# Optimization experiments

Hardware: AMD Instinct MI355X
Metric: run time of the kernel (lower is better)

The kernel has to match this reference:

```python
import jax, jax.numpy as jnp
import numpy as np

TEMP_LEN = 16
TARGET_LEN = 22
DIM = 768
HEADS = 12
B = 16
NT = TEMP_LEN * TEMP_LEN          # 256 template tokens
NG = TARGET_LEN * TARGET_LEN      # 484 target tokens
N = NT + NG                       # 740
POS_HID = 512


def _gaussian_heatmap(center, size, sig=1.0):
    x_axis = np.linspace(0, size[0] - 1, size[0]) - center[0]
    y_axis = np.linspace(0, size[1] - 1, size[1]) - center[1]
    xx, yy = np.meshgrid(x_axis, y_axis)
    return np.exp(-0.5 * (xx ** 2 + yy ** 2) / sig ** 2)


def _bias_index(L):
    # faithful to getBiasIndex (w_len == h_len here)
    coords = np.stack(np.meshgrid(np.arange(L), np.arange(L), indexing='ij'))  # [2,L,L]
    flat = coords.reshape(2, -1)                                               # [2,L*L]
    rel = (flat[:, :, None] - flat[:, None, :]).transpose(1, 2, 0).astype(np.int64)
    rel[:, :, 0] += L - 1
    rel[:, :, 1] += L - 1
    rel[:, :, 0] *= 2 * L - 1
    return rel.sum(-1)  # [L*L, L*L]


def setup_inputs() -> dict:
    key = jax.random.key(0)
    ks = jax.random.split(key, 12)
    f32 = jnp.float32
    x = jax.random.normal(ks[0], (B, N, DIM), dtype=f32)
    temp_q = jax.random.normal(ks[1], (B, NT, DIM), dtype=f32)
    target_q = jax.random.normal(ks[2], (B, NG, DIM), dtype=f32)
    # linear weights stored [in, out] (transposed torch layout)
    w = lambda k, i, o: jax.random.normal(k, (i, o), dtype=f32) * 0.02
    q_w = w(ks[3], DIM, DIM)
    k_w = w(ks[4], DIM, DIM)
    v_w = w(ks[5], DIM, DIM)
    proj_w = w(ks[6], DIM, DIM)
    proj_b = jnp.zeros((DIM,), dtype=f32)
    rpb_table = jax.random.normal(ks[7], ((2 * TARGET_LEN - 1) ** 2, HEADS), dtype=f32) * 0.0002
    rpb_table_temp = jax.random.normal(ks[8], ((2 * TEMP_LEN - 1) ** 2, HEADS), dtype=f32) * 0.0002
    pos_w1 = w(ks[9], 2, POS_HID)
    pos_b1 = jnp.zeros((POS_HID,), dtype=f32)
    pos_w2 = w(ks[10], POS_HID, HEADS)
    pos_b2 = jnp.zeros((HEADS,), dtype=f32)
    # deterministic cross-bias coordinate table (non-learned buffer)
    temp_tab = _gaussian_heatmap((TEMP_LEN // 2, TEMP_LEN // 2), (TEMP_LEN, TEMP_LEN)).astype(np.float32).flatten() \
        + np.linspace(-0.2, 0.2, NT, dtype=np.float32)
    targ_tab = _gaussian_heatmap((TARGET_LEN // 2, TARGET_LEN // 2), (TARGET_LEN, TARGET_LEN)).astype(np.float32).flatten() \
        + np.linspace(-0.2, 0.2, NG, dtype=np.float32)
    # torch.meshgrid default indexing='ij': [2, NT, NG] -> permute(1,2,0) -> [NT,NG,2]
    temp_target = np.stack(np.meshgrid(temp_tab, targ_tab, indexing='ij')).transpose(1, 2, 0)
    target_temp_tab = jnp.asarray(temp_target.transpose(1, 0, 2))  # [NG, NT, 2]
    temp_idx = jnp.asarray(_bias_index(TEMP_LEN))       # [NT, NT] int64
    target_idx = jnp.asarray(_bias_index(TARGET_LEN))   # [NG, NG] int64
    return {
        'x': x, 'temp_q': temp_q, 'target_q': target_q,
        'q_w': q_w, 'k_w': k_w, 'v_w': v_w, 'proj_w': proj_w, 'proj_b': proj_b,
        'rpb_table': rpb_table, 'rpb_table_temp': rpb_table_temp,
        'pos_w1': pos_w1, 'pos_b1': pos_b1, 'pos_w2': pos_w2, 'pos_b2': pos_b2,
        'target_temp_tab': target_temp_tab,
        'temp_idx': temp_idx, 'target_idx': target_idx,
    }


def reference(x, temp_q, target_q, q_w, k_w, v_w, proj_w, proj_b,
              rpb_table, rpb_table_temp, pos_w1, pos_b1, pos_w2, pos_b2,
              target_temp_tab, temp_idx, target_idx):
    Bsz, Ntok, C = x.shape
    H = HEADS
    hd = C // H
    scale = hd ** -0.5

    q_in = jnp.concatenate([temp_q, target_q], axis=1)                 # [B,N,C]
    q = (q_in @ q_w).reshape(Bsz, Ntok, H, hd).transpose(0, 2, 1, 3)   # [B,H,N,hd]
    k = (x @ k_w).reshape(Bsz, Ntok, H, hd).transpose(0, 2, 1, 3)
    v = (x @ v_w).reshape(Bsz, Ntok, H, hd).transpose(0, 2, 1, 3)

    # gathered relative position biases -> [H, Ni, Ni]
    temp_rpb = rpb_table_temp[temp_idx.reshape(-1)].reshape(NT, NT, H).transpose(2, 0, 1)
    targ_rpb = rpb_table[target_idx.reshape(-1)].reshape(NG, NG, H).transpose(2, 0, 1)
    # MLP cross bias: [NG, NT, 2] -> [NG, NT, H] -> [H, NG, NT]
    hid = jax.nn.relu(target_temp_tab @ pos_w1 + pos_b1)
    target_temp_bias = (hid @ pos_w2 + pos_b2).transpose(2, 0, 1)      # [H,NG,NT]
    temp_target_bias = target_temp_bias.transpose(0, 2, 1)             # [H,NT,NG]
    top = jnp.concatenate([temp_rpb, temp_target_bias], axis=2)        # [H,NT,N]
    bot = jnp.concatenate([target_temp_bias, targ_rpb], axis=2)        # [H,NG,N]
    bias = jnp.concatenate([top, bot], axis=1)[None]                   # [1,H,N,N]

    attn = jnp.einsum('bhnd,bhmd->bhnm', q, k) * scale + bias
    attn = jax.nn.softmax(attn, axis=-1)
    out = jnp.einsum('bhnm,bhmd->bhnd', attn, v).transpose(0, 2, 1, 3).reshape(Bsz, Ntok, C)
    return out @ proj_w + proj_b
```

## Files before the change

kernel.cpp:

```cpp
#include <hip/hip_runtime.h>


typedef unsigned short u16;
typedef short bf16x8 __attribute__((ext_vector_type(8)));
typedef float f32x4 __attribute__((ext_vector_type(4)));

#define BSZ   16
#define NTOK  740
#define NTMP  256
#define NTGT  484
#define DIMC  768
#define NHEAD 12
#define HDIM  64
#define MROWS (BSZ*NTOK)
#define SMAX  16.0f
#define VSTR  66

__device__ __forceinline__ float bf2f(u16 u) {
    return __uint_as_float(((unsigned int)u) << 16);
}
__device__ __forceinline__ float bflo(unsigned int u) {
    return __uint_as_float(u << 16);
}
__device__ __forceinline__ float bfhi(unsigned int u) {
    return __uint_as_float(u & 0xffff0000u);
}
__device__ __forceinline__ u16 f2bf(float f) {
    unsigned int u = __float_as_uint(f);
    u += 0x7fffu + ((u >> 16) & 1u);
    return (u16)(u >> 16);
}

__device__ __forceinline__ void gl_lds16(const u16* g, u16* l) {
    __builtin_amdgcn_global_load_lds(
        (const __attribute__((address_space(1))) unsigned int*)(unsigned long long)g,
        (__attribute__((address_space(3))) unsigned int*)(unsigned int)(unsigned long long)l,
        16, 0, 0);
}

__device__ __forceinline__ size_t b2off(int h, int i, int j) {
    return ((size_t)(h * NTOK + i)) * 768 + ((j >> 6) << 6) + ((j & 15) << 2) + ((j >> 4) & 3);
}

__global__ __launch_bounds__(256) void convert_qx(
    const float* __restrict__ x, const float* __restrict__ tq,
    const float* __restrict__ gq, u16* __restrict__ XB, u16* __restrict__ QB)
{
    int c = blockIdx.x * 256 + threadIdx.x;
    if (c >= MROWS * DIMC / 8) return;
    {
        const float* s = x + (size_t)c * 8;
        float4 p0 = *(const float4*)s, p1 = *(const float4*)(s + 4);
        u16 e[8] = {f2bf(p0.x), f2bf(p0.y), f2bf(p0.z), f2bf(p0.w),
                    f2bf(p1.x), f2bf(p1.y), f2bf(p1.z), f2bf(p1.w)};
        *(uint4*)(XB + (size_t)c * 8) = *(uint4*)e;
    }
    {
        int row = c / 96, cc = (c - row * 96) * 8;
        int b = row / NTOK, n = row - b * NTOK;
        const float* s = (n < NTMP)
                       ? tq + ((size_t)(b * NTMP + n)) * DIMC + cc
                       : gq + ((size_t)(b * NTGT + (n - NTMP))) * DIMC + cc;
        float4 p0 = *(const float4*)s, p1 = *(const float4*)(s + 4);
        u16 e[8] = {f2bf(p0.x), f2bf(p0.y), f2bf(p0.z), f2bf(p0.w),
                    f2bf(p1.x), f2bf(p1.y), f2bf(p1.z), f2bf(p1.w)};
        *(uint4*)(QB + (size_t)row * DIMC + cc) = *(uint4*)e;
    }
}

__global__ __launch_bounds__(256) void transpose_w(
    const float* __restrict__ w0, const float* __restrict__ w1,
    const float* __restrict__ w2, const float* __restrict__ w3,
    u16* __restrict__ Wt)
{
    __shared__ float T[64][65];
    const float* src = (blockIdx.z == 0) ? w0 : (blockIdx.z == 1) ? w1
                     : (blockIdx.z == 2) ? w2 : w3;
    const float scale = (blockIdx.z == 0) ? 0.125f : 1.0f;
    u16* dst = Wt + (size_t)blockIdx.z * DIMC * DIMC;
    int out0 = blockIdx.x * 64, in0 = blockIdx.y * 64;
    int tid = threadIdx.x;
    #pragma unroll
    for (int l = 0; l < 4; l++) {
        int u = tid + (l << 8);
        int r = u >> 4, c4 = (u & 15) << 2;
        float4 p = *(const float4*)(src + (size_t)(in0 + r) * DIMC + out0 + c4);
        T[r][c4] = p.x; T[r][c4 + 1] = p.y; T[r][c4 + 2] = p.z; T[r][c4 + 3] = p.w;
    }
    __syncthreads();
    #pragma unroll
    for (int l = 0; l < 2; l++) {
        int u = tid + (l << 8);
        int r = u >> 3, c8 = (u & 7) << 3;
        u16 e[8];
        #pragma unroll
        for (int i = 0; i < 8; i++) e[i] = f2bf(T[c8 + i][r] * scale);
        *(uint4*)(dst + (size_t)(out0 + r) * DIMC + in0 + c8) = *(uint4*)e;
    }
}

__global__ __launch_bounds__(256) void bias_diag(
    const float* __restrict__ rpb, const float* __restrict__ rpbt,
    const int* __restrict__ tidx, const int* __restrict__ gidx,
    u16* __restrict__ bias)
{
    int j = blockIdx.x * 256 + threadIdx.x;
    int i = blockIdx.y;
    if (j >= 768) return;
    u16 vals[NHEAD];
    if (j >= NTOK) {
        u16 neg = f2bf(-1e30f);
        #pragma unroll
        for (int h = 0; h < NHEAD; h++) vals[h] = neg;
    } else if (i < NTMP && j < NTMP) {
        int idx = tidx[i * NTMP + j];
        #pragma unroll
        for (int h = 0; h < NHEAD; h++) vals[h] = f2bf(rpbt[idx * NHEAD + h]);
    } else if (i >= NTMP && j >= NTMP) {
        int idx = gidx[(i - NTMP) * NTGT + (j - NTMP)];
        #pragma unroll
        for (int h = 0; h < NHEAD; h++) vals[h] = f2bf(rpb[idx * NHEAD + h]);
    } else {
        return;
    }
    #pragma unroll
    for (int h = 0; h < NHEAD; h++) bias[b2off(h, i, j)] = vals[h];
}

__global__ __launch_bounds__(256) void bias_cross(
    const float* __restrict__ w1, const float* __restrict__ b1,
    const float* __restrict__ w2, const float* __restrict__ b2,
    const float* __restrict__ tab, u16* __restrict__ bias)
{
    int g = blockIdx.x, t = threadIdx.x;
    float a  = tab[(g * NTMP + t) * 2 + 0];
    float bb = tab[(g * NTMP + t) * 2 + 1];
    float acc[NHEAD];
    #pragma unroll
    for (int h = 0; h < NHEAD; h++) acc[h] = b2[h];
    for (int k = 0; k < 512; k++) {
        float hid = fmaxf(a * w1[k] + bb * w1[512 + k] + b1[k], 0.0f);
        #pragma unroll
        for (int h = 0; h < NHEAD; h++) acc[h] += hid * w2[k * NHEAD + h];
    }
    #pragma unroll
    for (int h = 0; h < NHEAD; h++) {
        u16 v = f2bf(acc[h]);
        bias[b2off(h, t, NTMP + g)] = v;
        bias[b2off(h, NTMP + g, t)] = v;
    }
}

template<int MODE>
__global__ __launch_bounds__(256) void gemm_bf16(
    const u16* __restrict__ A, const u16* __restrict__ Wt,
    const float* __restrict__ pb, u16* __restrict__ C0,
    u16* __restrict__ C1, float* __restrict__ Cf)
{
    __shared__ __align__(16) u16 As[8192];
    __shared__ __align__(16) u16 Bs[8192];
    const int tid = threadIdx.x;
    const int lane = tid & 63, w = tid >> 6;
    const int quad = lane >> 4, ln = lane & 15;
    const int m0 = blockIdx.y << 7, n0g = blockIdx.x << 7;
    const int wm = (w >> 1) << 6, wn = (w & 1) << 6;
    const u16* Wbase = Wt + (size_t)n0g * DIMC;

    f32x4 acc[4][4];
    #pragma unroll
    for (int i = 0; i < 4; i++)
        #pragma unroll
        for (int j = 0; j < 4; j++)
            acc[i][j] = (f32x4){0.f, 0.f, 0.f, 0.f};

    for (int k0 = 0; k0 < DIMC; k0 += 64) {
        __syncthreads();
        #pragma unroll
        for (int l = 0; l < 4; l++) {
            int f = tid + (l << 8);
            int c8 = f >> 7, r = f & 127;
            int grow = m0 + r; if (grow >= MROWS) grow = MROWS - 1;
            gl_lds16(A + (size_t)grow * DIMC + k0 + c8 * 8, As + f * 8);
            gl_lds16(Wbase + (size_t)r * DIMC + k0 + c8 * 8, Bs + f * 8);
        }
        __syncthreads();
        #pragma unroll
        for (int kp = 0; kp < 2; kp++) {
            bf16x8 af[4], bfr[4];
            #pragma unroll
            for (int mt = 0; mt < 4; mt++)
                af[mt] = *(const bf16x8*)&As[(((kp << 2) + quad) * 128 + wm + mt * 16 + ln) * 8];
            #pragma unroll
            for (int nt = 0; nt < 4; nt++)
                bfr[nt] = *(const bf16x8*)&Bs[(((kp << 2) + quad) * 128 + wn + nt * 16 + ln) * 8];
            #pragma unroll
            for (int mt = 0; mt < 4; mt++)
                #pragma unroll
                for (int nt = 0; nt < 4; nt++)
                    acc[mt][nt] = __builtin_amdgcn_mfma_f32_16x16x32_bf16(
                        af[mt], bfr[nt], acc[mt][nt], 0, 0, 0);
        }
    }

    u16* Cb = C0;
    int col0 = n0g;
    if (MODE == 1 && n0g >= DIMC) { Cb = C1; col0 = n0g - DIMC; }

    #pragma unroll
    for (int mt = 0; mt < 4; mt++) {
        #pragma unroll
        for (int reg = 0; reg < 4; reg++) {
            int grow = m0 + wm + mt * 16 + (quad << 2) + reg;
            if (grow >= MROWS) continue;
            #pragma unroll
            for (int nt = 0; nt < 4; nt++) {
                int gcol = col0 + wn + nt * 16 + ln;
                float v = acc[mt][nt][reg];
                if (MODE == 2) {
                    Cf[(size_t)grow * DIMC + gcol] = v + pb[gcol];
                } else {
                    Cb[(size_t)grow * DIMC + gcol] = f2bf(v);
                }
            }
        }
    }
}

__global__ __launch_bounds__(256) void attn_mfma(
    const u16* __restrict__ Qg, const u16* __restrict__ Kg,
    const u16* __restrict__ Vg, const u16* __restrict__ bias,
    u16* __restrict__ ctx)
{
    __shared__ __align__(16) u16 KsL[4096];
    __shared__ __align__(16) u16 VtL[64 * VSTR];
    __shared__ __align__(16) u16 Pw[8][16][72];

    const int tid = threadIdx.x;
    const int lane = tid & 63, w = tid >> 6;
    const int quad = lane >> 4, ln = lane & 15;
    const int b = blockIdx.z, h = blockIdx.y;
    const int q0 = blockIdx.x << 7;
    const int mbase = q0 + (w << 5);
    const u16* bp = bias + ((size_t)h * NTOK) * 768;

    bf16x8 aq[2][2];
    #pragma unroll
    for (int mi = 0; mi < 2; mi++) {
        int qrow = mbase + (mi << 4) + ln; if (qrow >= NTOK) qrow = NTOK - 1;
        #pragma unroll
        for (int kp = 0; kp < 2; kp++)
            aq[mi][kp] = *(const bf16x8*)(Qg + ((size_t)(b * NTOK + qrow)) * DIMC
                                          + h * HDIM + kp * 32 + (quad << 3));
    }
    int boff[2][4];
    #pragma unroll
    for (int mi = 0; mi < 2; mi++)
        #pragma unroll
        for (int reg = 0; reg < 4; reg++) {
            int rr = mbase + (mi << 4) + (quad << 2) + reg;
            if (rr >= NTOK) rr = NTOK - 1;
            boff[mi][reg] = rr * 768 + (ln << 2);
        }

    float rs[2][4] = {};
    f32x4 O[2][4];
    #pragma unroll
    for (int mi = 0; mi < 2; mi++)
        #pragma unroll
        for (int dt = 0; dt < 4; dt++) O[mi][dt] = (f32x4){0.f, 0.f, 0.f, 0.f};

    for (int j0 = 0; j0 < NTOK; j0 += 64) {
        __syncthreads();
        #pragma unroll
        for (int l = 0; l < 2; l++) {
            int f = tid + (l << 8);
            int chunk = f >> 6, jr = f & 63;
            int krow = j0 + jr; if (krow >= NTOK) krow = NTOK - 1;
            gl_lds16(Kg + ((size_t)(b * NTOK + krow)) * DIMC + h * HDIM + chunk * 8,
                     KsL + f * 8);
        }
        uint2 bvv[2][4];
        #pragma unroll
        for (int mi = 0; mi < 2; mi++)
            #pragma unroll
            for (int reg = 0; reg < 4; reg++)
                bvv[mi][reg] = *(const uint2*)(bp + boff[mi][reg] + j0);
        #pragma unroll
        for (int l = 0; l < 2; l++) {
            int u = tid + (l << 8);
            int jr = u >> 3, d0 = (u & 7) << 3;
            int vrow = j0 + jr; if (vrow >= NTOK) vrow = NTOK - 1;
            uint4 p = *(const uint4*)(Vg + ((size_t)(b * NTOK + vrow)) * DIMC + h * HDIM + d0);
            const u16* pe = (const u16*)&p;
            #pragma unroll
            for (int i = 0; i < 8; i++) VtL[(d0 + i) * VSTR + jr] = pe[i];
        }
        __syncthreads();

        bf16x8 bv[4][2];
        #pragma unroll
        for (int dt = 0; dt < 4; dt++)
            #pragma unroll
            for (int kp = 0; kp < 2; kp++) {
                const unsigned int* vp = (const unsigned int*)
                    &VtL[(dt * 16 + ln) * VSTR + kp * 32 + (quad << 3)];
                uint4 vv; vv.x = vp[0]; vv.y = vp[1]; vv.z = vp[2]; vv.w = vp[3];
                bv[dt][kp] = *(const bf16x8*)&vv;
            }

        #pragma unroll
        for (int mi = 0; mi < 2; mi++) {
            f32x4 s[4];
            #pragma unroll
            for (int nt = 0; nt < 4; nt++) {
                f32x4 c = (f32x4){0.f, 0.f, 0.f, 0.f};
                #pragma unroll
                for (int kp = 0; kp < 2; kp++) {
                    bf16x8 bk = *(const bf16x8*)
                        &KsL[(((kp << 2) + quad) * 64 + nt * 16 + ln) * 8];
                    c = __builtin_amdgcn_mfma_f32_16x16x32_bf16(aq[mi][kp], bk, c, 0, 0, 0);
                }
                s[nt] = c;
            }
            #pragma unroll
            for (int reg = 0; reg < 4; reg++) {
                uint2 bb = bvv[mi][reg];
                float p0 = __expf(s[0][reg] + bflo(bb.x) - SMAX);
                float p1 = __expf(s[1][reg] + bfhi(bb.x) - SMAX);
                float p2 = __expf(s[2][reg] + bflo(bb.y) - SMAX);
                float p3 = __expf(s[3][reg] + bfhi(bb.y) - SMAX);
                s[0][reg] = p0; s[1][reg] = p1; s[2][reg] = p2; s[3][reg] = p3;
                rs[mi][reg] += p0 + p1 + p2 + p3;
            }
            #pragma unroll
            for (int nt = 0; nt < 4; nt++)
                #pragma unroll
                for (int reg = 0; reg < 4; reg++)
                    Pw[(w << 1) + mi][(quad << 2) + reg][nt * 16 + ln] = f2bf(s[nt][reg]);
            bf16x8 ap[2];
            #pragma unroll
            for (int kp = 0; kp < 2; kp++)
                ap[kp] = *(const bf16x8*)&Pw[(w << 1) + mi][ln][kp * 32 + (quad << 3)];
            #pragma unroll
            for (int dt = 0; dt < 4; dt++)
                #pragma unroll
                for (int kp = 0; kp < 2; kp++)
                    O[mi][dt] = __builtin_amdgcn_mfma_f32_16x16x32_bf16(
                        ap[kp], bv[dt][kp], O[mi][dt], 0, 0, 0);
        }
    }

    #pragma unroll
    for (int mi = 0; mi < 2; mi++) {
        #pragma unroll
        for (int reg = 0; reg < 4; reg++) {
            float t = rs[mi][reg];
            #pragma unroll
            for (int mk = 8; mk >= 1; mk >>= 1) t += __shfl_xor(t, mk);
            float inv = 1.0f / t;
            int row = mbase + (mi << 4) + (quad << 2) + reg;
            if (row < NTOK) {
                #pragma unroll
                for (int dt = 0; dt < 4; dt++)
                    ctx[((size_t)(b * NTOK + row)) * DIMC + h * HDIM + dt * 16 + ln]
                        = f2bf(O[mi][dt][reg] * inv);
            }
        }
    }
}

extern "C" void kernel_launch(void* const* d_in, const int* in_sizes, int n_in,
                              void* d_out, int out_size, void* d_ws, size_t ws_size,
                              hipStream_t stream)
{
    const float* x        = (const float*)d_in[0];
    const float* temp_q   = (const float*)d_in[1];
    const float* target_q = (const float*)d_in[2];
    const float* q_w      = (const float*)d_in[3];
    const float* k_w      = (const float*)d_in[4];
    const float* v_w      = (const float*)d_in[5];
    const float* proj_w   = (const float*)d_in[6];
    const float* proj_b   = (const float*)d_in[7];
    const float* rpb      = (const float*)d_in[8];
    const float* rpbt     = (const float*)d_in[9];
    const float* pw1      = (const float*)d_in[10];
    const float* pb1      = (const float*)d_in[11];
    const float* pw2      = (const float*)d_in[12];
    const float* pb2      = (const float*)d_in[13];
    const float* tab      = (const float*)d_in[14];
    const int*   tidx     = (const int*)d_in[15];
    const int*   gidx     = (const int*)d_in[16];
    float* out = (float*)d_out;

    char* ws = (char*)d_ws;
    const size_t S = (size_t)MROWS * DIMC * sizeof(u16);
    const size_t SZB = (size_t)NHEAD * NTOK * 768 * sizeof(u16);
    u16* XB    = (u16*)(ws);
    u16* QB    = (u16*)(ws + S);
    u16* Q     = (u16*)(ws + 2 * S);
    u16* K     = (u16*)(ws + 3 * S);
    u16* V     = QB;
    u16* CTX   = XB;
    u16* BIAS2 = (u16*)(ws + 4 * S);
    u16* WT    = (u16*)(ws + 4 * S + SZB);

    convert_qx<<<dim3(4440), 256, 0, stream>>>(x, temp_q, target_q, XB, QB);
    transpose_w<<<dim3(12, 12, 4), 256, 0, stream>>>(q_w, k_w, v_w, proj_w, WT);
    bias_diag<<<dim3(3, 740), 256, 0, stream>>>(rpb, rpbt, tidx, gidx, BIAS2);
    bias_cross<<<dim3(484), 256, 0, stream>>>(pw1, pb1, pw2, pb2, tab, BIAS2);

    const u16* WTq = WT;
    const u16* WTkv = WT + (size_t)DIMC * DIMC;
    const u16* WTp = WT + 3 * (size_t)DIMC * DIMC;

    gemm_bf16<0><<<dim3(6, 93), 256, 0, stream>>>(QB, WTq, nullptr, Q, nullptr, nullptr);
    gemm_bf16<1><<<dim3(12, 93), 256, 0, stream>>>(XB, WTkv, nullptr, K, V, nullptr);
    attn_mfma<<<dim3(6, 12, 16), 256, 0, stream>>>(Q, K, V, BIAS2, CTX);
    gemm_bf16<2><<<dim3(6, 93), 256, 0, stream>>>(CTX, WTp, proj_b, nullptr, nullptr, out);
}
```

Measured before the change: 506.4 us.

## Fuse prep kernels, swizzle attention LDS layouts, and batch QK MFMAs

Merges the four preprocessing kernels (input conversion, weight transpose, diagonal bias, cross bias MLP) into one launch, with block ranges picking the job. In the attention kernel, the V-transpose and P staging buffers get XOR-swizzled layouts so reads can be single 16-byte vector loads without bank conflicts. QK^T is also computed for both row tiles together so each K fragment load feeds two MFMAs. The GEMM output-pointer selection moves before the main loop. The fused prep kernel may have uneven block workloads, and the swizzle math adds some index arithmetic.

```diff
diff --git a/kernel.cpp b/kernel.cpp
--- a/kernel.cpp
+++ b/kernel.cpp
@@ -14,7 +14,6 @@
 #define HDIM  64
 #define MROWS (BSZ*NTOK)
 #define SMAX  16.0f
-#define VSTR  66
 
 __device__ __forceinline__ float bf2f(u16 u) {
     return __uint_as_float(((unsigned int)u) << 16);
@@ -42,112 +41,113 @@
     return ((size_t)(h * NTOK + i)) * 768 + ((j >> 6) << 6) + ((j & 15) << 2) + ((j >> 4) & 3);
 }
 
-__global__ __launch_bounds__(256) void convert_qx(
+#define PREP_CONV 4440
+#define PREP_TRW  (PREP_CONV + 576)
+#define PREP_DIAG (PREP_TRW + 2220)
+#define PREP_ALL  (PREP_DIAG + 484)
+
+__global__ __launch_bounds__(256) void prep_kernel(
     const float* __restrict__ x, const float* __restrict__ tq,
-    const float* __restrict__ gq, u16* __restrict__ XB, u16* __restrict__ QB)
-{
-    int c = blockIdx.x * 256 + threadIdx.x;
-    if (c >= MROWS * DIMC / 8) return;
-    {
-        const float* s = x + (size_t)c * 8;
-        float4 p0 = *(const float4*)s, p1 = *(const float4*)(s + 4);
-        u16 e[8] = {f2bf(p0.x), f2bf(p0.y), f2bf(p0.z), f2bf(p0.w),
-                    f2bf(p1.x), f2bf(p1.y), f2bf(p1.z), f2bf(p1.w)};
-        *(uint4*)(XB + (size_t)c * 8) = *(uint4*)e;
-    }
-    {
-        int row = c / 96, cc = (c - row * 96) * 8;
-        int b = row / NTOK, n = row - b * NTOK;
-        const float* s = (n < NTMP)
-                       ? tq + ((size_t)(b * NTMP + n)) * DIMC + cc
-                       : gq + ((size_t)(b * NTGT + (n - NTMP))) * DIMC + cc;
-        float4 p0 = *(const float4*)s, p1 = *(const float4*)(s + 4);
-        u16 e[8] = {f2bf(p0.x), f2bf(p0.y), f2bf(p0.z), f2bf(p0.w),
-                    f2bf(p1.x), f2bf(p1.y), f2bf(p1.z), f2bf(p1.w)};
-        *(uint4*)(QB + (size_t)row * DIMC + cc) = *(uint4*)e;
-    }
-}
-
-__global__ __launch_bounds__(256) void transpose_w(
+    const float* __restrict__ gq, u16* __restrict__ XB, u16* __restrict__ QB,
     const float* __restrict__ w0, const float* __restrict__ w1,
     const float* __restrict__ w2, const float* __restrict__ w3,
-    u16* __restrict__ Wt)
+    u16* __restrict__ Wt,
+    const float* __restrict__ rpb, const float* __restrict__ rpbt,
+    const int* __restrict__ tidx, const int* __restrict__ gidx,
+    const float* __restrict__ pw1, const float* __restrict__ pb1,
+    const float* __restrict__ pw2, const float* __restrict__ pb2,
+    const float* __restrict__ tab, u16* __restrict__ bias)
 {
     __shared__ float T[64][65];
-    const float* src = (blockIdx.z == 0) ? w0 : (blockIdx.z == 1) ? w1
-                     : (blockIdx.z == 2) ? w2 : w3;
-    const float scale = (blockIdx.z == 0) ? 0.125f : 1.0f;
-    u16* dst = Wt + (size_t)blockIdx.z * DIMC * DIMC;
-    int out0 = blockIdx.x * 64, in0 = blockIdx.y * 64;
-    int tid = threadIdx.x;
-    #pragma unroll
-    for (int l = 0; l < 4; l++) {
-        int u = tid + (l << 8);
-        int r = u >> 4, c4 = (u & 15) << 2;
-        float4 p = *(const float4*)(src + (size_t)(in0 + r) * DIMC + out0 + c4);
-        T[r][c4] = p.x; T[r][c4 + 1] = p.y; T[r][c4 + 2] = p.z; T[r][c4 + 3] = p.w;
-    }
-    __syncthreads();
-    #pragma unroll
-    for (int l = 0; l < 2; l++) {
-        int u = tid + (l << 8);
-        int r = u >> 3, c8 = (u & 7) << 3;
-        u16 e[8];
-        #pragma unroll
-        for (int i = 0; i < 8; i++) e[i] = f2bf(T[c8 + i][r] * scale);
-        *(uint4*)(dst + (size_t)(out0 + r) * DIMC + in0 + c8) = *(uint4*)e;
-    }
-}
-
-__global__ __launch_bounds__(256) void bias_diag(
-    const float* __restrict__ rpb, const float* __restrict__ rpbt,
-    const int* __restrict__ tidx, const int* __restrict__ gidx,
-    u16* __restrict__ bias)
-{
-    int j = blockIdx.x * 256 + threadIdx.x;
-    int i = blockIdx.y;
-    if (j >= 768) return;
-    u16 vals[NHEAD];
-    if (j >= NTOK) {
-        u16 neg = f2bf(-1e30f);
-        #pragma unroll
-        for (int h = 0; h < NHEAD; h++) vals[h] = neg;
-    } else if (i < NTMP && j < NTMP) {
-        int idx = tidx[i * NTMP + j];
-        #pragma unroll
-        for (int h = 0; h < NHEAD; h++) vals[h] = f2bf(rpbt[idx * NHEAD + h]);
-    } else if (i >= NTMP && j >= NTMP) {
-        int idx = gidx[(i - NTMP) * NTGT + (j - NTMP)];
-        #pragma unroll
-        for (int h = 0; h < NHEAD; h++) vals[h] = f2bf(rpb[idx * NHEAD + h]);
+    const int blk = blockIdx.x;
+    const int tid = threadIdx.x;
+
+    if (blk < PREP_CONV) {
+        int c = blk * 256 + tid;
+        {
+            const float* s = x + (size_t)c * 8;
+            float4 p0 = *(const float4*)s, p1 = *(const float4*)(s + 4);
+            u16 e[8] = {f2bf(p0.x), f2bf(p0.y), f2bf(p0.z), f2bf(p0.w),
+                        f2bf(p1.x), f2bf(p1.y), f2bf(p1.z), f2bf(p1.w)};
+            *(uint4*)(XB + (size_t)c * 8) = *(uint4*)e;
+        }
+        {
+            int row = c / 96, cc = (c - row * 96) * 8;
+            int b = row / NTOK, n = row - b * NTOK;
+            const float* s = (n < NTMP)
+                           ? tq + ((size_t)(b * NTMP + n)) * DIMC + cc
+                           : gq + ((size_t)(b * NTGT + (n - NTMP))) * DIMC + cc;
+            float4 p0 = *(const float4*)s, p1 = *(const float4*)(s + 4);
+            u16 e[8] = {f2bf(p0.x), f2bf(p0.y), f2bf(p0.z), f2bf(p0.w),
+                        f2bf(p1.x), f2bf(p1.y), f2bf(p1.z), f2bf(p1.w)};
+            *(uint4*)(QB + (size_t)row * DIMC + cc) = *(uint4*)e;
+        }
+    } else if (blk < PREP_TRW) {
+        int t = blk - PREP_CONV;
+        int z = t / 144, rem = t - z * 144;
+        int bx = rem % 12, by = rem / 12;
+        const float* src = (z == 0) ? w0 : (z == 1) ? w1 : (z == 2) ? w2 : w3;
+        const float scale = (z == 0) ? 0.125f : 1.0f;
+        u16* dst = Wt + (size_t)z * DIMC * DIMC;
+        int out0 = bx * 64, in0 = by * 64;
+        #pragma unroll
+        for (int l = 0; l < 4; l++) {
+            int u = tid + (l << 8);
+            int r = u >> 4, c4 = (u & 15) << 2;
+            float4 p = *(const float4*)(src + (size_t)(in0 + r) * DIMC + out0 + c4);
+            T[r][c4] = p.x; T[r][c4 + 1] = p.y; T[r][c4 + 2] = p.z; T[r][c4 + 3] = p.w;
+        }
+        __syncthreads();
+        #pragma unroll
+        for (int l = 0; l < 2; l++) {
+            int u = tid + (l << 8);
+            int r = u >> 3, c8 = (u & 7) << 3;
+            u16 e[8];
+            #pragma unroll
+            for (int i = 0; i < 8; i++) e[i] = f2bf(T[c8 + i][r] * scale);
+            *(uint4*)(dst + (size_t)(out0 + r) * DIMC + in0 + c8) = *(uint4*)e;
+        }
+    } else if (blk < PREP_DIAG) {
+        int t = blk - PREP_TRW;
+        int jb = t % 3, i = t / 3;
+        int j = jb * 256 + tid;
+        u16 vals[NHEAD];
+        if (j >= NTOK) {
+            u16 neg = f2bf(-1e30f);
+            #pragma unroll
+            for (int h = 0; h < NHEAD; h++) vals[h] = neg;
+        } else if (i < NTMP && j < NTMP) {
+            int idx = tidx[i * NTMP + j];
+            #pragma unroll
+            for (int h = 0; h < NHEAD; h++) vals[h] = f2bf(rpbt[idx * NHEAD + h]);
+        } else if (i >= NTMP && j >= NTMP) {
+            int idx = gidx[(i - NTMP) * NTGT + (j - NTMP)];
+            #pragma unroll
+            for (int h = 0; h < NHEAD; h++) vals[h] = f2bf(rpb[idx * NHEAD + h]);
+        } else {
+            return;
+        }
+        #pragma unroll
+        for (int h = 0; h < NHEAD; h++) bias[b2off(h, i, j)] = vals[h];
     } else {
-        return;
-    }
-    #pragma unroll
-    for (int h = 0; h < NHEAD; h++) bias[b2off(h, i, j)] = vals[h];
-}
-
-__global__ __launch_bounds__(256) void bias_cross(
-    const float* __restrict__ w1, const float* __restrict__ b1,
-    const float* __restrict__ w2, const float* __restrict__ b2,
-    const float* __restrict__ tab, u16* __restrict__ bias)
-{
-    int g = blockIdx.x, t = threadIdx.x;
-    float a  = tab[(g * NTMP + t) * 2 + 0];
-    float bb = tab[(g * NTMP + t) * 2 + 1];
-    float acc[NHEAD];
-    #pragma unroll
-    for (int h = 0; h < NHEAD; h++) acc[h] = b2[h];
-    for (int k = 0; k < 512; k++) {
-        float hid = fmaxf(a * w1[k] + bb * w1[512 + k] + b1[k], 0.0f);
-        #pragma unroll
-        for (int h = 0; h < NHEAD; h++) acc[h] += hid * w2[k * NHEAD + h];
-    }
-    #pragma unroll
-    for (int h = 0; h < NHEAD; h++) {
-        u16 v = f2bf(acc[h]);
-        bias[b2off(h, t, NTMP + g)] = v;
-        bias[b2off(h, NTMP + g, t)] = v;
+        int g = blk - PREP_DIAG;
+        int t = tid;
+        float a  = tab[(g * NTMP + t) * 2 + 0];
+        float bb = tab[(g * NTMP + t) * 2 + 1];
+        float acc[NHEAD];
+        #pragma unroll
+        for (int h = 0; h < NHEAD; h++) acc[h] = pb2[h];
+        for (int k = 0; k < 512; k++) {
+            float hid = fmaxf(a * pw1[k] + bb * pw1[512 + k] + pb1[k], 0.0f);
+            #pragma unroll
+            for (int h = 0; h < NHEAD; h++) acc[h] += hid * pw2[k * NHEAD + h];
+        }
+        #pragma unroll
+        for (int h = 0; h < NHEAD; h++) {
+            u16 v = f2bf(acc[h]);
+            bias[b2off(h, t, NTMP + g)] = v;
+            bias[b2off(h, NTMP + g, t)] = v;
+        }
     }
 }
 
@@ -162,9 +162,19 @@
     const int tid = threadIdx.x;
     const int lane = tid & 63, w = tid >> 6;
     const int quad = lane >> 4, ln = lane & 15;
-    const int m0 = blockIdx.y << 7, n0g = blockIdx.x << 7;
+    const int m0 = blockIdx.y << 7;
     const int wm = (w >> 1) << 6, wn = (w & 1) << 6;
-    const u16* Wbase = Wt + (size_t)n0g * DIMC;
+
+    const int nn = blockIdx.x << 7;
+    const u16* Wbase = Wt + (size_t)nn * DIMC;
+    u16* Cb;
+    int col0;
+    if (MODE == 1) {
+        if (nn < DIMC) { col0 = nn; Cb = C0; }
+        else           { col0 = nn - DIMC; Cb = C1; }
+    } else {
+        col0 = nn; Cb = C0;
+    }
 
     f32x4 acc[4][4];
     #pragma unroll
@@ -201,10 +211,6 @@
                         af[mt], bfr[nt], acc[mt][nt], 0, 0, 0);
         }
     }
-
-    u16* Cb = C0;
-    int col0 = n0g;
-    if (MODE == 1 && n0g >= DIMC) { Cb = C1; col0 = n0g - DIMC; }
 
     #pragma unroll
     for (int mt = 0; mt < 4; mt++) {
@@ -232,7 +238,7 @@
     u16* __restrict__ ctx)
 {
     __shared__ __align__(16) u16 KsL[4096];
-    __shared__ __align__(16) u16 VtL[64 * VSTR];
+    __shared__ __align__(16) u16 VtL[64 * 72];
     __shared__ __align__(16) u16 Pw[8][16][72];
 
     const int tid = threadIdx.x;
@@ -262,6 +268,8 @@
             boff[mi][reg] = rr * 768 + (ln << 2);
         }
 
+    const int pswz = ((ln >> 2) & 3) << 4;
+
     float rs[2][4] = {};
     f32x4 O[2][4];
     #pragma unroll
@@ -292,55 +300,65 @@
             int vrow = j0 + jr; if (vrow >= NTOK) vrow = NTOK - 1;
             uint4 p = *(const uint4*)(Vg + ((size_t)(b * NTOK + vrow)) * DIMC + h * HDIM + d0);
             const u16* pe = (const u16*)&p;
-            #pragma unroll
-            for (int i = 0; i < 8; i++) VtL[(d0 + i) * VSTR + jr] = pe[i];
+            int jswz = jr ^ d0;
+            #pragma unroll
+            for (int i = 0; i < 8; i++) VtL[(d0 + i) * 72 + jswz] = pe[i];
         }
         __syncthreads();
 
         bf16x8 bv[4][2];
         #pragma unroll
-        for (int dt = 0; dt < 4; dt++)
+        for (int dt = 0; dt < 4; dt++) {
+            int key8 = ((dt * 2 + (ln >> 3)) & 7) << 3;
             #pragma unroll
             for (int kp = 0; kp < 2; kp++) {
-                const unsigned int* vp = (const unsigned int*)
-                    &VtL[(dt * 16 + ln) * VSTR + kp * 32 + (quad << 3)];
-                uint4 vv; vv.x = vp[0]; vv.y = vp[1]; vv.z = vp[2]; vv.w = vp[3];
-                bv[dt][kp] = *(const bf16x8*)&vv;
+                int koff = (kp * 32 + (quad << 3)) ^ key8;
+                bv[dt][kp] = *(const bf16x8*)&VtL[(dt * 16 + ln) * 72 + koff];
+            }
+        }
+
+        f32x4 s[2][4];
+        #pragma unroll
+        for (int mi = 0; mi < 2; mi++)
+            #pragma unroll
+            for (int nt = 0; nt < 4; nt++) s[mi][nt] = (f32x4){0.f, 0.f, 0.f, 0.f};
+        #pragma unroll
+        for (int kp = 0; kp < 2; kp++)
+            #pragma unroll
+            for (int nt = 0; nt < 4; nt++) {
+                bf16x8 bk = *(const bf16x8*)
+                    &KsL[(((kp << 2) + quad) * 64 + nt * 16 + ln) * 8];
+                s[0][nt] = __builtin_amdgcn_mfma_f32_16x16x32_bf16(aq[0][kp], bk, s[0][nt], 0, 0, 0);
+                s[1][nt] = __builtin_amdgcn_mfma_f32_16x16x32_bf16(aq[1][kp], bk, s[1][nt], 0, 0, 0);
             }
 
         #pragma unroll
         for (int mi = 0; mi < 2; mi++) {
-            f32x4 s[4];
-            #pragma unroll
-            for (int nt = 0; nt < 4; nt++) {
-                f32x4 c = (f32x4){0.f, 0.f, 0.f, 0.f};
-                #pragma unroll
-                for (int kp = 0; kp < 2; kp++) {
-                    bf16x8 bk = *(const bf16x8*)
-                        &KsL[(((kp << 2) + quad) * 64 + nt * 16 + ln) * 8];
-                    c = __builtin_amdgcn_mfma_f32_16x16x32_bf16(aq[mi][kp], bk, c, 0, 0, 0);
-                }
-                s[nt] = c;
-            }
             #pragma unroll
             for (int reg = 0; reg < 4; reg++) {
                 uint2 bb = bvv[mi][reg];
-                float p0 = __expf(s[0][reg] + bflo(bb.x) - SMAX);
-                float p1 = __expf(s[1][reg] + bfhi(bb.x) - SMAX);
-                float p2 = __expf(s[2][reg] + bflo(bb.y) - SMAX);
-                float p3 = __expf(s[3][reg] + bfhi(bb.y) - SMAX);
-                s[0][reg] = p0; s[1][reg] = p1; s[2][reg] = p2; s[3][reg] = p3;
+                float p0 = __expf(s[mi][0][reg] + bflo(bb.x) - SMAX);
+                float p1 = __expf(s[mi][1][reg] + bfhi(bb.x) - SMAX);
+                float p2 = __expf(s[mi][2][reg] + bflo(bb.y) - SMAX);
+                float p3 = __expf(s[mi][3][reg] + bfhi(bb.y) - SMAX);
+                s[mi][0][reg] = p0; s[mi][1][reg] = p1;
+                s[mi][2][reg] = p2; s[mi][3][reg] = p3;
                 rs[mi][reg] += p0 + p1 + p2 + p3;
             }
-            #pragma unroll
-            for (int nt = 0; nt < 4; nt++)
+            u16* pwb = &Pw[(w << 1) + mi][0][0];
+            #pragma unroll
+            for (int nt = 0; nt < 4; nt++) {
+                int colw = ((nt ^ quad) << 4) + ln;
                 #pragma unroll
                 for (int reg = 0; reg < 4; reg++)
-                    Pw[(w << 1) + mi][(quad << 2) + reg][nt * 16 + ln] = f2bf(s[nt][reg]);
+                    pwb[((quad << 2) + reg) * 72 + colw] = f2bf(s[mi][nt][reg]);
+            }
             bf16x8 ap[2];
             #pragma unroll
-            for (int kp = 0; kp < 2; kp++)
-                ap[kp] = *(const bf16x8*)&Pw[(w << 1) + mi][ln][kp * 32 + (quad << 3)];
+            for (int kp = 0; kp < 2; kp++) {
+                int koff = (kp * 32 + (quad << 3)) ^ pswz;
+                ap[kp] = *(const bf16x8*)&pwb[ln * 72 + koff];
+            }
             #pragma unroll
             for (int dt = 0; dt < 4; dt++)
                 #pragma unroll
@@ -404,17 +422,18 @@
     u16* BIAS2 = (u16*)(ws + 4 * S);
     u16* WT    = (u16*)(ws + 4 * S + SZB);
 
-    convert_qx<<<dim3(4440), 256, 0, stream>>>(x, temp_q, target_q, XB, QB);
-    transpose_w<<<dim3(12, 12, 4), 256, 0, stream>>>(q_w, k_w, v_w, proj_w, WT);
-    bias_diag<<<dim3(3, 740), 256, 0, stream>>>(rpb, rpbt, tidx, gidx, BIAS2);
-    bias_cross<<<dim3(484), 256, 0, stream>>>(pw1, pb1, pw2, pb2, tab, BIAS2);
+    prep_kernel<<<dim3(PREP_ALL), 256, 0, stream>>>(
+        x, temp_q, target_q, XB, QB,
+        q_w, k_w, v_w, proj_w, WT,
+        rpb, rpbt, tidx, gidx,
+        pw1, pb1, pw2, pb2, tab, BIAS2);
 
     const u16* WTq = WT;
-    const u16* WTkv = WT + (size_t)DIMC * DIMC;
+    const u16* WTk = WT + (size_t)DIMC * DIMC;
     const u16* WTp = WT + 3 * (size_t)DIMC * DIMC;
 
     gemm_bf16<0><<<dim3(6, 93), 256, 0, stream>>>(QB, WTq, nullptr, Q, nullptr, nullptr);
-    gemm_bf16<1><<<dim3(12, 93), 256, 0, stream>>>(XB, WTkv, nullptr, K, V, nullptr);
+    gemm_bf16<1><<<dim3(12, 93), 256, 0, stream>>>(XB, WTk, nullptr, K, V, nullptr);
     attn_mfma<<<dim3(6, 12, 16), 256, 0, stream>>>(Q, K, V, BIAS2, CTX);
     gemm_bf16<2><<<dim3(6, 93), 256, 0, stream>>>(CTX, WTp, proj_b, nullptr, nullptr, out);
 }
```

Result: faster. 495.8 us (-2.1%).
